# Performance work log

Hardware: AMD Instinct MI355X
Metric: run time of the kernel (lower is better)

Reference implementation:

```python
import jax, jax.numpy as jnp
import numpy as np

V, E, H, TAGS = 50000, 128, 128, 8  # H = hidden per direction (hidden_dim // 2)
B, T = 64, 512


def _lstm_dir(x, w_ih, w_hh, b_ih, b_hh, reverse):
    # x: [B,T,I] -> hs: [B,T,H]; PyTorch gate order i,f,g,o
    xg = jnp.einsum('bti,gi->btg', x, w_ih) + b_ih + b_hh  # [B,T,4H]
    if reverse:
        xg = xg[:, ::-1]
    Bn = x.shape[0]
    Hn = w_hh.shape[1]

    def step(carry, g):
        h, c = carry
        g = g + h @ w_hh.T
        i, f, gg, o = jnp.split(g, 4, axis=-1)
        c = jax.nn.sigmoid(f) * c + jax.nn.sigmoid(i) * jnp.tanh(gg)
        h = jax.nn.sigmoid(o) * jnp.tanh(c)
        return (h, c), h

    h0 = jnp.zeros((Bn, Hn), x.dtype)
    _, hs = jax.lax.scan(step, (h0, h0), jnp.swapaxes(xg, 0, 1))
    hs = jnp.swapaxes(hs, 0, 1)
    return hs[:, ::-1] if reverse else hs


def _crf_partition(emissions, transitions):
    # emissions: [B,T,K]; scan the forward algorithm over time
    fv0 = emissions[:, 0]  # [B,K]

    def step(fv, emit):
        fv = jax.nn.logsumexp(fv[:, :, None] + transitions[None] + emit[:, None, :], axis=1)
        return fv, None

    fv, _ = jax.lax.scan(step, fv0, jnp.swapaxes(emissions[:, 1:], 0, 1))
    return jax.nn.logsumexp(fv, axis=1)  # [B]


def _forward_nll(sentences, tags, embedding, lstm_params, h2t_w, h2t_b, transitions):
    x = embedding[sentences]  # [B,T,E]; dropout inactive (eval)
    for pf, pb in lstm_params:
        x = jnp.concatenate([_lstm_dir(x, *pf, False), _lstm_dir(x, *pb, True)], axis=-1)
    emissions = x @ h2t_w.T + h2t_b  # [B,T,K]
    # gold path score (mask = all ones)
    emit_score = jnp.take_along_axis(emissions, tags[:, :, None], axis=2)[..., 0].sum(axis=1)
    trans_score = transitions[tags[:, :-1], tags[:, 1:]].sum(axis=1)
    partition = _crf_partition(emissions, transitions)
    return -(emit_score + trans_score - partition).mean()


def setup_inputs() -> dict:
    key = jax.random.key(0)
    ks = jax.random.split(key, 40)
    sc = 0.05
    inp = {}
    inp['sentences'] = jax.random.randint(ks[0], (B, T), 0, V)
    inp['tags'] = jax.random.randint(ks[1], (B, T), 0, TAGS)
    emb = jax.random.normal(ks[2], (V, E), jnp.float32) * sc
    inp['embedding'] = emb.at[0].set(0.0)  # padding_idx=0
    idx = 3
    for l in range(2):
        in_dim = E if l == 0 else 2 * H
        for d in ('', '_rev'):
            inp[f'w_ih_l{l}{d}'] = jax.random.normal(ks[idx], (4 * H, in_dim), jnp.float32) * sc; idx += 1
            inp[f'w_hh_l{l}{d}'] = jax.random.normal(ks[idx], (4 * H, H), jnp.float32) * sc; idx += 1
            inp[f'b_ih_l{l}{d}'] = jax.random.normal(ks[idx], (4 * H,), jnp.float32) * sc; idx += 1
            inp[f'b_hh_l{l}{d}'] = jax.random.normal(ks[idx], (4 * H,), jnp.float32) * sc; idx += 1
    inp['h2t_w'] = jax.random.normal(ks[idx], (TAGS, 2 * H), jnp.float32) * sc; idx += 1
    inp['h2t_b'] = jax.random.normal(ks[idx], (TAGS,), jnp.float32) * sc; idx += 1
    trans = jax.random.normal(ks[idx], (TAGS, TAGS), jnp.float32)
    inp['transitions'] = trans.at[0, :].set(-10000.0).at[:, 0].set(-10000.0)
    return inp


def reference(sentences, tags, embedding,
              w_ih_l0, w_hh_l0, b_ih_l0, b_hh_l0,
              w_ih_l0_rev, w_hh_l0_rev, b_ih_l0_rev, b_hh_l0_rev,
              w_ih_l1, w_hh_l1, b_ih_l1, b_hh_l1,
              w_ih_l1_rev, w_hh_l1_rev, b_ih_l1_rev, b_hh_l1_rev,
              h2t_w, h2t_b, transitions):
    lstm_params = [
        ((w_ih_l0, w_hh_l0, b_ih_l0, b_hh_l0), (w_ih_l0_rev, w_hh_l0_rev, b_ih_l0_rev, b_hh_l0_rev)),
        ((w_ih_l1, w_hh_l1, b_ih_l1, b_hh_l1), (w_ih_l1_rev, w_hh_l1_rev, b_ih_l1_rev, b_hh_l1_rev)),
    ]
    return _forward_nll(sentences, tags, embedding, lstm_params, h2t_w, h2t_b, transitions)
```

## Files before the change

### kernel.cpp

```cpp
#include <hip/hip_runtime.h>
#include <cstdint>
#include <cstddef>

typedef __attribute__((ext_vector_type(8))) short bf16x8;
typedef __attribute__((ext_vector_type(8))) int   v8i;
typedef __attribute__((ext_vector_type(4))) float f32x4;

__device__ __forceinline__ unsigned short f2bf(float x) {
    union { float f; unsigned u; } v; v.f = x;
    unsigned r = (v.u + 0x7fffu + ((v.u >> 16) & 1u)) >> 16;
    return (unsigned short)r;
}
__device__ __forceinline__ float bflo(unsigned u){ union{unsigned i;float f;}v; v.i = u << 16;        return v.f; }
__device__ __forceinline__ float bfhi(unsigned u){ union{unsigned i;float f;}v; v.i = u & 0xffff0000u; return v.f; }
__device__ __forceinline__ float frcp(float x){ return __builtin_amdgcn_rcpf(x); }
__device__ __forceinline__ float fsig(float x){ return frcp(1.f + __expf(-x)); }
__device__ __forceinline__ float ftanh(float x){ return 2.f * frcp(1.f + __expf(-2.f * x)) - 1.f; }

#define BARRIER_LGKM() asm volatile("s_waitcnt lgkmcnt(0)\n\ts_barrier" ::: "memory")

#define BB 64
#define TT 512
#define MM (BB*TT)
#define NG 1024

__device__ __forceinline__ int perm_orig(int g2) {
    return (g2 & 3) * 128 + (g2 >> 6) * 16 + ((g2 >> 4) & 3) * 4 + ((g2 >> 2) & 3);
}

__global__ void prep_kernel(
    const int* __restrict__ sentences, const float* __restrict__ emb,
    const float* __restrict__ w_ih_l0, const float* __restrict__ w_ih_l0r,
    const float* __restrict__ w_ih_l1, const float* __restrict__ w_ih_l1r,
    const float* __restrict__ w_hh_l0, const float* __restrict__ w_hh_l0r,
    const float* __restrict__ w_hh_l1, const float* __restrict__ w_hh_l1r,
    const float* __restrict__ b_ih_l0, const float* __restrict__ b_hh_l0,
    const float* __restrict__ b_ih_l0r, const float* __restrict__ b_hh_l0r,
    const float* __restrict__ b_ih_l1, const float* __restrict__ b_hh_l1,
    const float* __restrict__ b_ih_l1r, const float* __restrict__ b_hh_l1r,
    unsigned short* __restrict__ x0, unsigned short* __restrict__ W0c,
    unsigned short* __restrict__ W1c,
    int* __restrict__ Whh0q, int* __restrict__ Whh1q,
    float* __restrict__ bias0, float* __restrict__ bias1)
{
    int blk = blockIdx.x;
    if (blk < 4096) {
        int t4 = blk * 256 + threadIdx.x;
        int e4 = t4 * 4; int m = e4 >> 7; int k = e4 & 127;
        int tt = m >> 6, b = m & 63;
        int s = sentences[b * 512 + tt];
        float4 v = *(const float4*)(emb + (size_t)s * 128 + k);
        *(ushort4*)(x0 + (size_t)m * 128 + k) =
            make_ushort4(f2bf(v.x), f2bf(v.y), f2bf(v.z), f2bf(v.w));
    } else if (blk < 4224) {
        int t4 = (blk - 4096) * 256 + threadIdx.x;
        int e4 = t4 * 4; int n = e4 >> 7; int k = e4 & 127;
        int dir = n >> 9; int orig = perm_orig(n & 511);
        const float* src = dir ? w_ih_l0r : w_ih_l0;
        float4 v = *(const float4*)(src + (size_t)orig * 128 + k);
        *(ushort4*)(W0c + (size_t)n * 128 + k) =
            make_ushort4(f2bf(v.x), f2bf(v.y), f2bf(v.z), f2bf(v.w));
    } else if (blk < 4480) {
        int t4 = (blk - 4224) * 256 + threadIdx.x;
        int e4 = t4 * 4; int n = e4 >> 8; int k = e4 & 255;
        int dir = n >> 9; int orig = perm_orig(n & 511);
        const float* src = dir ? w_ih_l1r : w_ih_l1;
        float4 v = *(const float4*)(src + (size_t)orig * 256 + k);
        *(ushort4*)(W1c + (size_t)n * 256 + k) =
            make_ushort4(f2bf(v.x), f2bf(v.y), f2bf(v.z), f2bf(v.w));
    } else if (blk < 4736) {
        int lb = blk - 4480;
        int layer = lb >> 7;
        int t4 = (lb & 127) * 256 + threadIdx.x;
        int f  = t4 * 4;
        int j0   = f & 31;
        int lp   = (f >> 5) & 63;
        int quad = lp >> 4, r = lp & 15;
        int tb   = f >> 11;
        int tile = tb & 3, w = (tb >> 2) & 7, dir = tb >> 5;
        int g2 = w * 64 + tile * 16 + r;
        int orig = perm_orig(g2);
        const float* src = layer ? (dir ? w_hh_l1r : w_hh_l1)
                                 : (dir ? w_hh_l0r : w_hh_l0);
        int k = quad * 32 + j0;
        float4 v = *(const float4*)(src + (size_t)orig * 128 + k);
        int p = __builtin_amdgcn_cvt_pk_fp8_f32(v.x * 64.f, v.y * 64.f, 0, false);
        p = __builtin_amdgcn_cvt_pk_fp8_f32(v.z * 64.f, v.w * 64.f, p, true);
        (layer ? Whh1q : Whh0q)[f >> 2] = p;
    } else {
        int t = (blk - 4736) * 256 + threadIdx.x;
        int n = t & 1023;
        int dir = n >> 9; int orig = perm_orig(n & 511);
        if (t < 1024)
            bias0[n] = dir ? (b_ih_l0r[orig] + b_hh_l0r[orig]) : (b_ih_l0[orig] + b_hh_l0[orig]);
        else
            bias1[n] = dir ? (b_ih_l1r[orig] + b_hh_l1r[orig]) : (b_ih_l1[orig] + b_hh_l1[orig]);
    }
}

__global__ __launch_bounds__(256, 2) void gemm_xg(
    const unsigned short* __restrict__ W,
    const unsigned short* __restrict__ X,
    const float* __restrict__ bias,
    unsigned short* __restrict__ xgS,
    int K)
{
    __shared__ unsigned short sW[128 * 32];
    __shared__ unsigned short sX[128 * 32];
    const int tid  = threadIdx.x;
    const int lane = tid & 63;
    const int wid  = tid >> 6;
    const int w_n  = wid & 1, w_m = wid >> 1;
    const int r16  = lane & 15, quad = lane >> 4;
    const int nTile = blockIdx.x * 128;
    const int mTile = blockIdx.y * 128;

    f32x4 zero = {0.f, 0.f, 0.f, 0.f};
    f32x4 acc[4][4];
    #pragma unroll
    for (int i = 0; i < 4; ++i)
        #pragma unroll
        for (int j = 0; j < 4; ++j) acc[i][j] = zero;

    const int q0 = tid, q1 = tid + 256;
    const int r0 = q0 >> 2, c0 = q0 & 3, ko0 = c0 * 8;
    const int r1 = q1 >> 2, c1 = q1 & 3, ko1 = c1 * 8;
    const int s0 = (r0 << 2) | (c0 ^ ((r0 >> 1) & 3));
    const int s1 = (r1 << 2) | (c1 ^ ((r1 >> 1) & 3));
    const int rsw = quad ^ ((r16 >> 1) & 3);

    const unsigned short* Wp0 = W + (size_t)(nTile + r0) * K + ko0;
    const unsigned short* Wp1 = W + (size_t)(nTile + r1) * K + ko1;
    const unsigned short* Xp0 = X + (size_t)(mTile + r0) * K + ko0;
    const unsigned short* Xp1 = X + (size_t)(mTile + r1) * K + ko1;

    uint4 wv0 = *(const uint4*)(Wp0);
    uint4 wv1 = *(const uint4*)(Wp1);
    uint4 xv0 = *(const uint4*)(Xp0);
    uint4 xv1 = *(const uint4*)(Xp1);

    for (int k0 = 0; k0 < K; k0 += 32) {
        BARRIER_LGKM();
        ((uint4*)sW)[s0] = wv0;
        ((uint4*)sW)[s1] = wv1;
        ((uint4*)sX)[s0] = xv0;
        ((uint4*)sX)[s1] = xv1;
        BARRIER_LGKM();
        if (k0 + 32 < K) {
            wv0 = *(const uint4*)(Wp0 + k0 + 32);
            wv1 = *(const uint4*)(Wp1 + k0 + 32);
            xv0 = *(const uint4*)(Xp0 + k0 + 32);
            xv1 = *(const uint4*)(Xp1 + k0 + 32);
        }
        const bf16x8* sWv = (const bf16x8*)sW;
        const bf16x8* sXv = (const bf16x8*)sX;
        bf16x8 a[4], bx[4];
        #pragma unroll
        for (int i = 0; i < 4; ++i) {
            a[i]  = sWv[((w_n * 64 + i * 16 + r16) << 2) | rsw];
            bx[i] = sXv[((w_m * 64 + i * 16 + r16) << 2) | rsw];
        }
        #pragma unroll
        for (int i = 0; i < 4; ++i)
            #pragma unroll
            for (int j = 0; j < 4; ++j)
                acc[i][j] = __builtin_amdgcn_mfma_f32_16x16x32_bf16(a[i], bx[j], acc[i][j], 0, 0, 0);
    }

    const int w_idx = ((nTile & 511) >> 6) + w_n;
    const int dirn  = nTile >> 9;
    float4 bv[4];
    #pragma unroll
    for (int i = 0; i < 4; ++i)
        bv[i] = *(const float4*)(bias + nTile + w_n * 64 + i * 16 + quad * 4);
    const int t  = (mTile >> 6) + w_m;
    const size_t pbase = (size_t)(t >> 1) * 131072 + (size_t)dirn * 65536
                       + (size_t)w_idx * 512 + (size_t)(t & 1) * 4;
    #pragma unroll
    for (int j = 0; j < 4; ++j) {
        int b = j * 16 + r16;
        size_t base = pbase + (size_t)(b >> 2) * 4096;
        #pragma unroll
        for (int i = 0; i < 4; ++i) {
            f32x4 v = acc[i][j];
            ushort4 o = make_ushort4(f2bf(v.x + bv[i].x), f2bf(v.y + bv[i].y),
                                     f2bf(v.z + bv[i].z), f2bf(v.w + bv[i].w));
            *(uint2*)(xgS + base + (size_t)(quad * 16 + i * 4 + (b & 3)) * 8) = *(uint2*)&o;
        }
    }
}

__global__ __launch_bounds__(512, 1) void lstm_scan_mfma(
    const unsigned short* __restrict__ xgS,
    const unsigned char* __restrict__ whh_q,
    unsigned short* __restrict__ xnext)
{
    const int dir = blockIdx.x >> 4;
    const int bg  = blockIdx.x & 15;
    const int tid = threadIdx.x;
    const int w   = tid >> 6;
    const int lane= tid & 63;
    const int q   = lane >> 4;
    const int bl  = lane & 15;
    const int d   = bl >> 2;
    const int b4  = bl & 3;
    const int u   = w * 16 + d * 4 + q;
    const int b   = bg * 4 + b4;

    v8i afrag[4];
    {
        const unsigned char* wb = whh_q + (size_t)dir * 65536 + (size_t)w * 8192 + lane * 32;
        #pragma unroll
        for (int tile = 0; tile < 4; ++tile) {
            uint4 a0 = *(const uint4*)(wb + tile * 2048);
            uint4 a1 = *(const uint4*)(wb + tile * 2048 + 16);
            v8i av; av[0]=a0.x; av[1]=a0.y; av[2]=a0.z; av[3]=a0.w;
                    av[4]=a1.x; av[5]=a1.y; av[6]=a1.z; av[7]=a1.w;
            afrag[tile] = av;
        }
    }

    __shared__ __align__(16) unsigned char hbuf[2][576];
    if (tid < 144) ((unsigned*)hbuf[1])[tid] = 0;

    float c = 0.f;
    const long pstep = dir ? -131072L : 131072L;
    const unsigned short* xp = xgS + (size_t)(dir ? 255 : 0) * 131072
                             + (size_t)dir * 65536 + bg * 4096 + w * 512 + lane * 8;
    const long hstep = dir ? -16384L : 16384L;
    long hoff = (long)(dir ? 511 : 0) * 16384 + (long)b * 256 + dir * 128 + u;

    const int hw  = b4 * 144 + u;
    const int hr  = b4 * 144 + q * 32;

    auto step_body = [&](uint2 xv, const unsigned char* rb, unsigned char* wbuf) {
        uint4 h0 = *(const uint4*)(rb + hr);
        uint4 h1 = *(const uint4*)(rb + hr + 16);
        v8i bfr; bfr[0]=h0.x; bfr[1]=h0.y; bfr[2]=h0.z; bfr[3]=h0.w;
                 bfr[4]=h1.x; bfr[5]=h1.y; bfr[6]=h1.z; bfr[7]=h1.w;
        f32x4 gv;
        gv.x = bflo(xv.x); gv.y = bfhi(xv.x);
        gv.z = bflo(xv.y); gv.w = bfhi(xv.y);
        f32x4 a0 = gv, a1 = gv, a2 = gv, a3 = gv;
        a0 = __builtin_amdgcn_mfma_scale_f32_16x16x128_f8f6f4(afrag[0], bfr, a0, 0, 0,
                 0, 0x79797979, 0, 0x7B7B7B7B);
        a1 = __builtin_amdgcn_mfma_scale_f32_16x16x128_f8f6f4(afrag[1], bfr, a1, 0, 0,
                 0, 0x79797979, 0, 0x7B7B7B7B);
        a2 = __builtin_amdgcn_mfma_scale_f32_16x16x128_f8f6f4(afrag[2], bfr, a2, 0, 0,
                 0, 0x79797979, 0, 0x7B7B7B7B);
        a3 = __builtin_amdgcn_mfma_scale_f32_16x16x128_f8f6f4(afrag[3], bfr, a3, 0, 0,
                 0, 0x79797979, 0, 0x7B7B7B7B);
        f32x4 sel = a0;
        sel = (d == 1) ? a1 : sel;
        sel = (d == 2) ? a2 : sel;
        sel = (d == 3) ? a3 : sel;
        float si = fsig(sel.x);
        float sf = fsig(sel.y);
        float tg = ftanh(sel.z);
        float so = fsig(sel.w);
        c = sf * c + si * tg;
        float h = so * ftanh(c);
        xnext[hoff] = f2bf(h);
        hoff += hstep;
        int q8 = __builtin_amdgcn_cvt_pk_fp8_f32(h * 16.f, h * 16.f, 0, false);
        wbuf[hw] = (unsigned char)(q8 & 0xff);
        BARRIER_LGKM();
    };

    uint4 ring[4];
    #pragma unroll
    for (int i = 0; i < 4; ++i)
        ring[i] = *(const uint4*)(xp + (long)i * pstep);

    BARRIER_LGKM();

    for (int it2 = 0; it2 < 64; ++it2) {
        #pragma unroll
        for (int pp = 0; pp < 4; ++pp) {
            uint4 rv = ring[pp];
            uint2 xa, xb;
            if (dir) { xa.x = rv.z; xa.y = rv.w; xb.x = rv.x; xb.y = rv.y; }
            else     { xa.x = rv.x; xa.y = rv.y; xb.x = rv.z; xb.y = rv.w; }
            ring[pp] = *(const uint4*)(xp + 4 * pstep);
            xp += pstep;
            step_body(xa, hbuf[1], hbuf[0]);
            step_body(xb, hbuf[0], hbuf[1]);
        }
    }
}

__global__ void emis_kernel(const unsigned short* __restrict__ x2,
                            const float* __restrict__ h2t_w,
                            const float* __restrict__ h2t_b,
                            float* __restrict__ emis)
{
    int idx = blockIdx.x * 256 + threadIdx.x;
    int m = idx >> 3, tag = idx & 7;
    const unsigned short* xr = x2 + (size_t)m * 256;
    const float* wr = h2t_w + (size_t)tag * 256;
    float a0 = 0.f, a1 = 0.f, a2 = 0.f, a3 = 0.f;
    #pragma unroll 4
    for (int k = 0; k < 256; k += 8) {
        uint4 xv = *(const uint4*)(xr + k);
        float4 w0 = *(const float4*)(wr + k);
        float4 w1 = *(const float4*)(wr + k + 4);
        a0 += bflo(xv.x) * w0.x + bfhi(xv.x) * w0.y;
        a1 += bflo(xv.y) * w0.z + bfhi(xv.y) * w0.w;
        a2 += bflo(xv.z) * w1.x + bfhi(xv.z) * w1.y;
        a3 += bflo(xv.w) * w1.z + bfhi(xv.w) * w1.w;
    }
    emis[idx] = h2t_b[tag] + ((a0 + a1) + (a2 + a3));
}

__global__ void crf_kernel(const float* __restrict__ emis,
                           const int* __restrict__ tags,
                           const float* __restrict__ trans,
                           float* __restrict__ partials)
{
    const int l = threadIdx.x;
    const int sl = l >> 3, j = l & 7, sl8 = sl * 8;
    const int b = blockIdx.x * 8 + sl;
    float T[8];
    #pragma unroll
    for (int i = 0; i < 8; ++i) T[i] = trans[i * 8 + j];

    const float* eb = emis + (size_t)b * 8 + j;
    float fv = eb[0];
    float e1 = eb[512], e2 = eb[1024];

    auto step = [&](float e_t) {
        float v0 = __shfl(fv, sl8 + 0) + T[0];
        float v1 = __shfl(fv, sl8 + 1) + T[1];
        float v2 = __shfl(fv, sl8 + 2) + T[2];
        float v3 = __shfl(fv, sl8 + 3) + T[3];
        float v4 = __shfl(fv, sl8 + 4) + T[4];
        float v5 = __shfl(fv, sl8 + 5) + T[5];
        float v6 = __shfl(fv, sl8 + 6) + T[6];
        float v7 = __shfl(fv, sl8 + 7) + T[7];
        float m = fmaxf(fmaxf(fmaxf(v0, v1), fmaxf(v2, v3)),
                        fmaxf(fmaxf(v4, v5), fmaxf(v6, v7)));
        float s = __expf(v0 - m) + __expf(v1 - m) + __expf(v2 - m) + __expf(v3 - m)
                + __expf(v4 - m) + __expf(v5 - m) + __expf(v6 - m) + __expf(v7 - m);
        fv = m + __logf(s) + e_t;
    };

    int t = 1;
    for (int it = 0; it < 255; ++it) {
        step(e1); e1 = eb[(size_t)(t + 2) * 512]; ++t;
        step(e2); e2 = eb[(size_t)(t + 2) * 512]; ++t;
    }
    step(e1);

    float m2 = fv;
    m2 = fmaxf(m2, __shfl_xor(m2, 1));
    m2 = fmaxf(m2, __shfl_xor(m2, 2));
    m2 = fmaxf(m2, __shfl_xor(m2, 4));
    float e2s = __expf(fv - m2);
    e2s += __shfl_xor(e2s, 1);
    e2s += __shfl_xor(e2s, 2);
    e2s += __shfl_xor(e2s, 4);
    float partition = m2 + __logf(e2s);

    const int* tg = tags + (size_t)b * TT;
    float sc = 0.f;
    for (int tt = j; tt < TT; tt += 8) {
        int tag = tg[tt];
        sc += emis[((size_t)tt * 64 + b) * 8 + tag];
        if (tt > 0) sc += trans[tg[tt - 1] * 8 + tag];
    }
    sc += __shfl_xor(sc, 1);
    sc += __shfl_xor(sc, 2);
    sc += __shfl_xor(sc, 4);
    if (j == 0) partials[b] = sc - partition;
}

__global__ void final_kernel(const float* __restrict__ partials, float* __restrict__ out)
{
    int l = threadIdx.x;
    float v = partials[l];
    #pragma unroll
    for (int d = 1; d < 64; d <<= 1) v += __shfl_xor(v, d);
    if (l == 0) out[0] = -v / 64.f;
}

extern "C" void kernel_launch(void* const* d_in, const int* in_sizes, int n_in,
                              void* d_out, int out_size, void* d_ws, size_t ws_size,
                              hipStream_t stream)
{
    const int*   sentences = (const int*)d_in[0];
    const int*   tags      = (const int*)d_in[1];
    const float* embedding = (const float*)d_in[2];
    const float* w_ih_l0   = (const float*)d_in[3];
    const float* w_hh_l0   = (const float*)d_in[4];
    const float* b_ih_l0   = (const float*)d_in[5];
    const float* b_hh_l0   = (const float*)d_in[6];
    const float* w_ih_l0r  = (const float*)d_in[7];
    const float* w_hh_l0r  = (const float*)d_in[8];
    const float* b_ih_l0r  = (const float*)d_in[9];
    const float* b_hh_l0r  = (const float*)d_in[10];
    const float* w_ih_l1   = (const float*)d_in[11];
    const float* w_hh_l1   = (const float*)d_in[12];
    const float* b_ih_l1   = (const float*)d_in[13];
    const float* b_hh_l1   = (const float*)d_in[14];
    const float* w_ih_l1r  = (const float*)d_in[15];
    const float* w_hh_l1r  = (const float*)d_in[16];
    const float* b_ih_l1r  = (const float*)d_in[17];
    const float* b_hh_l1r  = (const float*)d_in[18];
    const float* h2t_w     = (const float*)d_in[19];
    const float* h2t_b     = (const float*)d_in[20];
    const float* trans     = (const float*)d_in[21];

    char* ws = (char*)d_ws;
    unsigned short* W0c   = (unsigned short*)(ws + 0);
    unsigned short* W1c   = (unsigned short*)(ws + 262144);
    int*  Whh0q           = (int*)(ws + 786432);
    int*  Whh1q           = (int*)(ws + 917504);
    float* bias0          = (float*)(ws + 1310720);
    float* bias1          = (float*)(ws + 1314816);
    float* emis           = (float*)(ws + 1318912);
    float* partials       = (float*)(ws + 2375680);
    unsigned short* xgS   = (unsigned short*)(ws + 4194304);
    unsigned short* x0    = (unsigned short*)(ws + 71303168);
    unsigned short* x1    = (unsigned short*)(ws + 72351744);
    unsigned short* x2    = x1;
    (void)ws_size; (void)in_sizes; (void)n_in; (void)out_size;

    prep_kernel<<<4744, 256, 0, stream>>>(sentences, embedding,
        w_ih_l0, w_ih_l0r, w_ih_l1, w_ih_l1r,
        w_hh_l0, w_hh_l0r, w_hh_l1, w_hh_l1r,
        b_ih_l0, b_hh_l0, b_ih_l0r, b_hh_l0r,
        b_ih_l1, b_hh_l1, b_ih_l1r, b_hh_l1r,
        x0, W0c, W1c, Whh0q, Whh1q, bias0, bias1);

    gemm_xg<<<dim3(8, 256), 256, 0, stream>>>(W0c, x0, bias0, xgS, 128);
    lstm_scan_mfma<<<32, 512, 0, stream>>>(xgS, (const unsigned char*)Whh0q, x1);
    gemm_xg<<<dim3(8, 256), 256, 0, stream>>>(W1c, x1, bias1, xgS, 256);
    lstm_scan_mfma<<<32, 512, 0, stream>>>(xgS, (const unsigned char*)Whh1q, x2);
    emis_kernel<<<1024, 256, 0, stream>>>(x2, h2t_w, h2t_b, emis);
    crf_kernel<<<8, 64, 0, stream>>>(emis, tags, trans, partials);
    final_kernel<<<1, 64, 0, stream>>>(partials, (float*)d_out);
}
```

Baseline: 707.2 us.

## Chunk CRF forward scan across time and trim LSTM step critical path

The CRF forward recursion, which ran as 511 serial logsumexp steps in just 8 blocks, is split into 8 time chunks. Each chunk computes an 8x8 log-semiring transfer matrix in its own block (512 blocks in total), and a small combine kernel then chains the chunk matrices. In the LSTM scan step, the MFMAs now start from a zero accumulator so the xg load is off their dependency path, the h store uses truncation instead of round-to-nearest bf16, and pointer arithmetic is narrowed to int. This adds an extra kernel launch and a little more total CRF work, and truncating h slightly changes the numerics.

```diff
diff --git a/kernel.cpp b/kernel.cpp
--- a/kernel.cpp
+++ b/kernel.cpp
@@ -10,6 +10,10 @@
     union { float f; unsigned u; } v; v.f = x;
     unsigned r = (v.u + 0x7fffu + ((v.u >> 16) & 1u)) >> 16;
     return (unsigned short)r;
+}
+__device__ __forceinline__ unsigned short f2bf_trunc(float x) {
+    union { float f; unsigned u; } v; v.f = x;
+    return (unsigned short)(v.u >> 16);
 }
 __device__ __forceinline__ float bflo(unsigned u){ union{unsigned i;float f;}v; v.i = u << 16;        return v.f; }
 __device__ __forceinline__ float bfhi(unsigned u){ union{unsigned i;float f;}v; v.i = u & 0xffff0000u; return v.f; }
@@ -223,12 +227,14 @@
     __shared__ __align__(16) unsigned char hbuf[2][576];
     if (tid < 144) ((unsigned*)hbuf[1])[tid] = 0;
 
+    const f32x4 zero4 = {0.f, 0.f, 0.f, 0.f};
+
     float c = 0.f;
-    const long pstep = dir ? -131072L : 131072L;
+    const int pstep = dir ? -131072 : 131072;
     const unsigned short* xp = xgS + (size_t)(dir ? 255 : 0) * 131072
                              + (size_t)dir * 65536 + bg * 4096 + w * 512 + lane * 8;
-    const long hstep = dir ? -16384L : 16384L;
-    long hoff = (long)(dir ? 511 : 0) * 16384 + (long)b * 256 + dir * 128 + u;
+    const int hstep = dir ? -16384 : 16384;
+    unsigned short* hp = xnext + (size_t)(dir ? 511 : 0) * 16384 + b * 256 + dir * 128 + u;
 
     const int hw  = b4 * 144 + u;
     const int hr  = b4 * 144 + q * 32;
@@ -238,30 +244,30 @@
         uint4 h1 = *(const uint4*)(rb + hr + 16);
         v8i bfr; bfr[0]=h0.x; bfr[1]=h0.y; bfr[2]=h0.z; bfr[3]=h0.w;
                  bfr[4]=h1.x; bfr[5]=h1.y; bfr[6]=h1.z; bfr[7]=h1.w;
-        f32x4 gv;
-        gv.x = bflo(xv.x); gv.y = bfhi(xv.x);
-        gv.z = bflo(xv.y); gv.w = bfhi(xv.y);
-        f32x4 a0 = gv, a1 = gv, a2 = gv, a3 = gv;
-        a0 = __builtin_amdgcn_mfma_scale_f32_16x16x128_f8f6f4(afrag[0], bfr, a0, 0, 0,
-                 0, 0x79797979, 0, 0x7B7B7B7B);
-        a1 = __builtin_amdgcn_mfma_scale_f32_16x16x128_f8f6f4(afrag[1], bfr, a1, 0, 0,
-                 0, 0x79797979, 0, 0x7B7B7B7B);
-        a2 = __builtin_amdgcn_mfma_scale_f32_16x16x128_f8f6f4(afrag[2], bfr, a2, 0, 0,
-                 0, 0x79797979, 0, 0x7B7B7B7B);
-        a3 = __builtin_amdgcn_mfma_scale_f32_16x16x128_f8f6f4(afrag[3], bfr, a3, 0, 0,
-                 0, 0x79797979, 0, 0x7B7B7B7B);
+        f32x4 a0 = __builtin_amdgcn_mfma_scale_f32_16x16x128_f8f6f4(afrag[0], bfr, zero4, 0, 0,
+                       0, 0x79797979, 0, 0x7B7B7B7B);
+        f32x4 a1 = __builtin_amdgcn_mfma_scale_f32_16x16x128_f8f6f4(afrag[1], bfr, zero4, 0, 0,
+                       0, 0x79797979, 0, 0x7B7B7B7B);
+        f32x4 a2 = __builtin_amdgcn_mfma_scale_f32_16x16x128_f8f6f4(afrag[2], bfr, zero4, 0, 0,
+                       0, 0x79797979, 0, 0x7B7B7B7B);
+        f32x4 a3 = __builtin_amdgcn_mfma_scale_f32_16x16x128_f8f6f4(afrag[3], bfr, zero4, 0, 0,
+                       0, 0x79797979, 0, 0x7B7B7B7B);
         f32x4 sel = a0;
         sel = (d == 1) ? a1 : sel;
         sel = (d == 2) ? a2 : sel;
         sel = (d == 3) ? a3 : sel;
-        float si = fsig(sel.x);
-        float sf = fsig(sel.y);
-        float tg = ftanh(sel.z);
-        float so = fsig(sel.w);
+        float iv = sel.x + bflo(xv.x);
+        float fv = sel.y + bfhi(xv.x);
+        float gg = sel.z + bflo(xv.y);
+        float ov = sel.w + bfhi(xv.y);
+        float si = fsig(iv);
+        float sf = fsig(fv);
+        float tg = ftanh(gg);
+        float so = fsig(ov);
         c = sf * c + si * tg;
         float h = so * ftanh(c);
-        xnext[hoff] = f2bf(h);
-        hoff += hstep;
+        *hp = f2bf_trunc(h);
+        hp += hstep;
         int q8 = __builtin_amdgcn_cvt_pk_fp8_f32(h * 16.f, h * 16.f, 0, false);
         wbuf[hw] = (unsigned char)(q8 & 0xff);
         BARRIER_LGKM();
@@ -270,7 +276,7 @@
     uint4 ring[4];
     #pragma unroll
     for (int i = 0; i < 4; ++i)
-        ring[i] = *(const uint4*)(xp + (long)i * pstep);
+        ring[i] = *(const uint4*)(xp + i * pstep);
 
     BARRIER_LGKM();
 
@@ -312,44 +318,74 @@
     emis[idx] = h2t_b[tag] + ((a0 + a1) + (a2 + a3));
 }
 
-__global__ void crf_kernel(const float* __restrict__ emis,
-                           const int* __restrict__ tags,
-                           const float* __restrict__ trans,
-                           float* __restrict__ partials)
-{
+__global__ void crf_chunk(const float* __restrict__ emis,
+                          const float* __restrict__ trans,
+                          float* __restrict__ Pc)
+{
+    const int b = blockIdx.x >> 3;
+    const int cch = blockIdx.x & 7;
     const int l = threadIdx.x;
-    const int sl = l >> 3, j = l & 7, sl8 = sl * 8;
-    const int b = blockIdx.x * 8 + sl;
+    const int i = l >> 3, j = l & 7;
+    const int i8 = i * 8;
     float T[8];
     #pragma unroll
-    for (int i = 0; i < 8; ++i) T[i] = trans[i * 8 + j];
-
-    const float* eb = emis + (size_t)b * 8 + j;
-    float fv = eb[0];
-    float e1 = eb[512], e2 = eb[1024];
-
-    auto step = [&](float e_t) {
-        float v0 = __shfl(fv, sl8 + 0) + T[0];
-        float v1 = __shfl(fv, sl8 + 1) + T[1];
-        float v2 = __shfl(fv, sl8 + 2) + T[2];
-        float v3 = __shfl(fv, sl8 + 3) + T[3];
-        float v4 = __shfl(fv, sl8 + 4) + T[4];
-        float v5 = __shfl(fv, sl8 + 5) + T[5];
-        float v6 = __shfl(fv, sl8 + 6) + T[6];
-        float v7 = __shfl(fv, sl8 + 7) + T[7];
+    for (int k = 0; k < 8; ++k) T[k] = trans[k * 8 + j];
+
+    const int t0 = (cch == 0) ? 1 : cch * 64;
+    const int t1 = cch * 64 + 64;
+    const float* ej = emis + (size_t)b * 8 + j;
+
+    float P = trans[i * 8 + j] + ej[(size_t)t0 * 512];
+    float e1 = ej[(size_t)(t0 + 1) * 512];
+    for (int t = t0 + 1; t < t1; ++t) {
+        float v0 = __shfl(P, i8 + 0) + T[0];
+        float v1 = __shfl(P, i8 + 1) + T[1];
+        float v2 = __shfl(P, i8 + 2) + T[2];
+        float v3 = __shfl(P, i8 + 3) + T[3];
+        float v4 = __shfl(P, i8 + 4) + T[4];
+        float v5 = __shfl(P, i8 + 5) + T[5];
+        float v6 = __shfl(P, i8 + 6) + T[6];
+        float v7 = __shfl(P, i8 + 7) + T[7];
         float m = fmaxf(fmaxf(fmaxf(v0, v1), fmaxf(v2, v3)),
                         fmaxf(fmaxf(v4, v5), fmaxf(v6, v7)));
         float s = __expf(v0 - m) + __expf(v1 - m) + __expf(v2 - m) + __expf(v3 - m)
                 + __expf(v4 - m) + __expf(v5 - m) + __expf(v6 - m) + __expf(v7 - m);
-        fv = m + __logf(s) + e_t;
-    };
-
-    int t = 1;
-    for (int it = 0; it < 255; ++it) {
-        step(e1); e1 = eb[(size_t)(t + 2) * 512]; ++t;
-        step(e2); e2 = eb[(size_t)(t + 2) * 512]; ++t;
-    }
-    step(e1);
+        P = m + __logf(s) + e1;
+        e1 = ej[(size_t)(t + 1) * 512];
+    }
+    Pc[((size_t)b * 8 + cch) * 64 + l] = P;
+}
+
+__global__ void crf_combine(const float* __restrict__ emis,
+                            const float* __restrict__ Pc,
+                            const int* __restrict__ tags,
+                            const float* __restrict__ trans,
+                            float* __restrict__ partials)
+{
+    const int l = threadIdx.x;
+    const int sl = l >> 3, j = l & 7, sl8 = sl * 8;
+    const int b = blockIdx.x * 8 + sl;
+
+    float fv = emis[(size_t)b * 8 + j];
+    #pragma unroll
+    for (int cch = 0; cch < 8; ++cch) {
+        const float* Pb = Pc + ((size_t)b * 8 + cch) * 64 + j;
+        float p0 = Pb[0],  p1 = Pb[8],  p2 = Pb[16], p3 = Pb[24];
+        float p4 = Pb[32], p5 = Pb[40], p6 = Pb[48], p7 = Pb[56];
+        float v0 = __shfl(fv, sl8 + 0) + p0;
+        float v1 = __shfl(fv, sl8 + 1) + p1;
+        float v2 = __shfl(fv, sl8 + 2) + p2;
+        float v3 = __shfl(fv, sl8 + 3) + p3;
+        float v4 = __shfl(fv, sl8 + 4) + p4;
+        float v5 = __shfl(fv, sl8 + 5) + p5;
+        float v6 = __shfl(fv, sl8 + 6) + p6;
+        float v7 = __shfl(fv, sl8 + 7) + p7;
+        float m = fmaxf(fmaxf(fmaxf(v0, v1), fmaxf(v2, v3)),
+                        fmaxf(fmaxf(v4, v5), fmaxf(v6, v7)));
+        float s = __expf(v0 - m) + __expf(v1 - m) + __expf(v2 - m) + __expf(v3 - m)
+                + __expf(v4 - m) + __expf(v5 - m) + __expf(v6 - m) + __expf(v7 - m);
+        fv = m + __logf(s);
+    }
 
     float m2 = fv;
     m2 = fmaxf(m2, __shfl_xor(m2, 1));
@@ -419,6 +455,7 @@
     float* bias1          = (float*)(ws + 1314816);
     float* emis           = (float*)(ws + 1318912);
     float* partials       = (float*)(ws + 2375680);
+    float* Pc             = (float*)(ws + 2375936);
     unsigned short* xgS   = (unsigned short*)(ws + 4194304);
     unsigned short* x0    = (unsigned short*)(ws + 71303168);
     unsigned short* x1    = (unsigned short*)(ws + 72351744);
@@ -437,6 +474,7 @@
     gemm_xg<<<dim3(8, 256), 256, 0, stream>>>(W1c, x1, bias1, xgS, 256);
     lstm_scan_mfma<<<32, 512, 0, stream>>>(xgS, (const unsigned char*)Whh1q, x2);
     emis_kernel<<<1024, 256, 0, stream>>>(x2, h2t_w, h2t_b, emis);
-    crf_kernel<<<8, 64, 0, stream>>>(emis, tags, trans, partials);
+    crf_chunk<<<512, 64, 0, stream>>>(emis, trans, Pc);
+    crf_combine<<<8, 64, 0, stream>>>(emis, Pc, tags, trans, partials);
     final_kernel<<<1, 64, 0, stream>>>(partials, (float*)d_out);
 }
```

Result: faster. 645.5 us (-8.7%).
